# Optimization experiments

Measured on AMD Instinct MI355X. Metric: run time of the kernel, lower is better.

The kernel has to match this reference:

```python
import jax, jax.numpy as jnp
import numpy as np

N = 196608   # total bonds in batch
H = 256      # hidden_size
NH = 8       # num_heads
D = H // NH  # att_size = 32
S = 4096     # num molecules (segments)
EPS = 1e-5


def setup_inputs() -> dict:
    key = jax.random.key(0)
    ks = jax.random.split(key, 12)
    f32 = jnp.float32
    return {
        "message": jax.random.normal(ks[0], (N, H), f32),
        "W_q": jax.random.normal(ks[1], (H, H), f32) * 0.05,
        "W_k": jax.random.normal(ks[2], (H, H), f32) * 0.05,
        "W_v": jax.random.normal(ks[3], (H, H), f32) * 0.05,
        "W_r": jax.random.normal(ks[4], (D, D), f32) * 0.15,
        "w_alpha": jax.random.normal(ks[5], (D,), f32),
        "w_beta": jax.random.normal(ks[6], (D,), f32),
        "W_o": jax.random.normal(ks[7], (H, H), f32) * 0.05,
        "b_o": jax.random.normal(ks[8], (H,), f32) * 0.02,
        "gamma": 1.0 + 0.1 * jax.random.normal(ks[9], (H,), f32),
        "beta_ln": 0.1 * jax.random.normal(ks[10], (H,), f32),
        "segment_ids": jnp.sort(jax.random.randint(ks[11], (N,), 0, S, dtype=jnp.int32)),
        "num_segments": S,
    }


def reference(message, W_q, W_k, W_v, W_r, w_alpha, w_beta, W_o, b_o,
              gamma, beta_ln, segment_ids, num_segments):
    scale = D ** (-0.5)
    # projections (torch Linear: y = x @ W.T), split heads -> [N, NH, D]
    q = (message @ W_q.T).reshape(-1, NH, D)
    k = (message @ W_k.T).reshape(-1, NH, D)
    v = (message @ W_v.T).reshape(-1, NH, D)
    # additive attention: softmax over feature dim d (per bond, per head)
    alpha = jax.nn.softmax(q * w_alpha * scale, axis=-1)
    # global query: sum over bonds within each molecule -> [S, NH, D]
    gq = jax.ops.segment_sum(alpha * q, segment_ids, num_segments=num_segments)
    p = gq[segment_ids] * k                      # [N, NH, D]
    beta = jax.nn.softmax(p * w_beta * scale, axis=-1)
    gk = jax.ops.segment_sum(beta * p, segment_ids, num_segments=num_segments)
    kvi = gk[segment_ids] * v                    # key-value interaction [N, NH, D]
    out = jnp.einsum('nhd,ed->nhe', kvi, W_r) + q  # weight_r on d, residual with q
    out = jax.nn.relu(out)                       # chemprop ReLU activation; dropout p=0
    out = out.reshape(-1, NH * D)
    out = out @ W_o.T + b_o
    # LayerNorm over hidden dim
    mu = jnp.mean(out, axis=-1, keepdims=True)
    var = jnp.mean(jnp.square(out - mu), axis=-1, keepdims=True)
    out = (out - mu) * jax.lax.rsqrt(var + EPS) * gamma + beta_ln
    # prepend cached zero vector (padding row), as the torch loop does for i == 0
    zero = jnp.zeros((1, H), dtype=out.dtype)
    return jnp.concatenate([zero, out], axis=0)
```

## Files before the change

kernel.cpp:

```cpp
#include <hip/hip_runtime.h>
#include <hip/hip_bf16.h>

#define N_BONDS 196608
#define HID     256
#define NSEG    4096
#define SMSCALE 0.17677669529663687f
#define LN_EPS  1e-5f
#define CHUNK   8

typedef __hip_bfloat16 bf16;
typedef __attribute__((ext_vector_type(8))) short short8_t;
typedef __attribute__((ext_vector_type(4))) float f32x4_t;

__device__ __forceinline__ float bf2f(bf16 x) { return __bfloat162float(x); }
__device__ __forceinline__ short f2bs(float f) {
    union { bf16 b; short s; } cv; cv.b = __float2bfloat16(f); return cv.s;
}
__device__ __forceinline__ float us2f(ushort u) {
    union { ushort u; bf16 b; } cv; cv.u = u; return __bfloat162float(cv.b);
}

__device__ __forceinline__ float gsum32(float x) {
#pragma unroll
    for (int m = 16; m >= 1; m >>= 1) x += __shfl_xor(x, m);
    return x;
}

__global__ void cast_kernel(const float* __restrict__ src, ushort* __restrict__ dst, int n4) {
    int i = blockIdx.x * blockDim.x + threadIdx.x;
    const int stride = gridDim.x * blockDim.x;
    for (; i < n4; i += stride) {
        float4 v = reinterpret_cast<const float4*>(src)[i];
        union { ushort4 u; bf16 b[4]; } cv;
        cv.b[0] = __float2bfloat16(v.x);
        cv.b[1] = __float2bfloat16(v.y);
        cv.b[2] = __float2bfloat16(v.z);
        cv.b[3] = __float2bfloat16(v.w);
        reinterpret_cast<ushort4*>(dst)[i] = cv.u;
    }
}

template <typename OutT>
__global__ __launch_bounds__(256, 2) void gemm_bt(const ushort* __restrict__ A,
                                                  const ushort* __restrict__ W,
                                                  OutT* __restrict__ C) {
    __shared__ __align__(16) char lds[128 * 512];
    const int t = threadIdx.x;
    const int colhalf = blockIdx.y;
#pragma unroll
    for (int it = 0; it < 16; ++it) {
        int c = it * 256 + t;
        int j = c >> 5, kc = c & 31;
        uint4 val = *reinterpret_cast<const uint4*>(W + ((colhalf << 7) + j) * HID + (kc << 3));
        *reinterpret_cast<uint4*>(lds + j * 512 + ((kc << 4) ^ ((j & 7) << 4))) = val;
    }
    __syncthreads();

    const int wave = t >> 6, lane = t & 63;
    const int lr = lane & 15, lk = lane >> 4;
    const long rowbase = (long)blockIdx.x * 128 + wave * 32;

    f32x4_t acc[2][8];
#pragma unroll
    for (int r = 0; r < 2; ++r)
#pragma unroll
        for (int cc = 0; cc < 8; ++cc) acc[r][cc] = (f32x4_t){0.f, 0.f, 0.f, 0.f};

    const ushort* a0 = A + (rowbase + lr) * HID;
    const ushort* a1 = a0 + 16 * HID;
#pragma unroll
    for (int k0 = 0; k0 < HID; k0 += 32) {
        const int koff = k0 + lk * 8;
        short8_t af0 = *reinterpret_cast<const short8_t*>(a0 + koff);
        short8_t af1 = *reinterpret_cast<const short8_t*>(a1 + koff);
#pragma unroll
        for (int cc = 0; cc < 8; ++cc) {
            const int j = cc * 16 + lr;
            short8_t bfr = *reinterpret_cast<const short8_t*>(
                lds + j * 512 + (((k0 << 1) + (lk << 4)) ^ ((j & 7) << 4)));
            acc[0][cc] = __builtin_amdgcn_mfma_f32_16x16x32_bf16(af0, bfr, acc[0][cc], 0, 0, 0);
            acc[1][cc] = __builtin_amdgcn_mfma_f32_16x16x32_bf16(af1, bfr, acc[1][cc], 0, 0, 0);
        }
    }
#pragma unroll
    for (int r = 0; r < 2; ++r) {
#pragma unroll
        for (int cc = 0; cc < 8; ++cc) {
            const int col = (colhalf << 7) + cc * 16 + lr;
#pragma unroll
            for (int reg = 0; reg < 4; ++reg) {
                const long row = rowbase + r * 16 + lk * 4 + reg;
                const float v = acc[r][cc][reg];
                if constexpr (sizeof(OutT) == 2) C[row * HID + col] = __float2bfloat16(v);
                else                             C[row * HID + col] = v;
            }
        }
    }
}

__global__ __launch_bounds__(256) void alpha_gq_kernel(const bf16* __restrict__ qb,
                                                       const float* __restrict__ w_alpha,
                                                       const int* __restrict__ seg,
                                                       float* __restrict__ gq) {
    const int j = threadIdx.x;
    const float wa = w_alpha[j & 31] * SMSCALE;
    const long n0 = (long)blockIdx.x * CHUNK;
    float acc = 0.f;
    int cur = -1;
    for (int i = 0; i < CHUNK; ++i) {
        const long n = n0 + i;
        const int s = seg[n];
        const float qv = bf2f(qb[n * HID + j]);
        const float e = __expf(qv * wa);
        const float ssum = gsum32(e);
        const float alpha = e / ssum;
        if (s != cur) {
            if (cur >= 0) atomicAdd(&gq[(long)cur * HID + j], acc);
            acc = 0.f;
            cur = s;
        }
        acc += alpha * qv;
    }
    atomicAdd(&gq[(long)cur * HID + j], acc);
}

__global__ __launch_bounds__(256) void beta_gk_kernel(const bf16* __restrict__ kb,
                                                      const float* __restrict__ gq,
                                                      const float* __restrict__ w_beta,
                                                      const int* __restrict__ seg,
                                                      float* __restrict__ gk) {
    const int j = threadIdx.x;
    const float wb = w_beta[j & 31] * SMSCALE;
    const long n0 = (long)blockIdx.x * CHUNK;
    float acc = 0.f;
    int cur = -1;
    for (int i = 0; i < CHUNK; ++i) {
        const long n = n0 + i;
        const int s = seg[n];
        const float kv = bf2f(kb[n * HID + j]);
        const float p = gq[(long)s * HID + j] * kv;
        const float e = __expf(p * wb);
        const float ssum = gsum32(e);
        const float beta = e / ssum;
        if (s != cur) {
            if (cur >= 0) atomicAdd(&gk[(long)cur * HID + j], acc);
            acc = 0.f;
            cur = s;
        }
        acc += beta * p;
    }
    atomicAdd(&gk[(long)cur * HID + j], acc);
}

__global__ __launch_bounds__(256) void act_exact_kernel(const ushort* __restrict__ vb,
                                                        const ushort* __restrict__ qb,
                                                        const float* __restrict__ gk,
                                                        const float* __restrict__ Wr,
                                                        const int* __restrict__ seg,
                                                        ushort* __restrict__ act) {
    __shared__ __align__(16) float wr_lds[1024];
    const int t = threadIdx.x;
#pragma unroll
    for (int i = 0; i < 4; ++i) wr_lds[i * 256 + t] = Wr[i * 256 + t];
    __syncthreads();

    const long tid = (long)blockIdx.x * 256 + t;
    const int n = (int)(tid >> 3), h = (int)(tid & 7);
    const int sid = seg[n];

    const float* gp = gk + (long)sid * HID + h * 32;
    const ushort* vp = vb + tid * 32;
    float kvi[32];
#pragma unroll
    for (int dq = 0; dq < 4; ++dq) {
        short8_t v8 = *reinterpret_cast<const short8_t*>(vp + dq * 8);
        float4 ga = reinterpret_cast<const float4*>(gp)[dq * 2];
        float4 gb = reinterpret_cast<const float4*>(gp)[dq * 2 + 1];
        kvi[dq * 8 + 0] = ga.x * us2f((ushort)v8[0]);
        kvi[dq * 8 + 1] = ga.y * us2f((ushort)v8[1]);
        kvi[dq * 8 + 2] = ga.z * us2f((ushort)v8[2]);
        kvi[dq * 8 + 3] = ga.w * us2f((ushort)v8[3]);
        kvi[dq * 8 + 4] = gb.x * us2f((ushort)v8[4]);
        kvi[dq * 8 + 5] = gb.y * us2f((ushort)v8[5]);
        kvi[dq * 8 + 6] = gb.z * us2f((ushort)v8[6]);
        kvi[dq * 8 + 7] = gb.w * us2f((ushort)v8[7]);
    }

    const ushort* qp = qb + tid * 32;
    short8_t q8[4];
#pragma unroll
    for (int i = 0; i < 4; ++i) q8[i] = *reinterpret_cast<const short8_t*>(qp + i * 8);

    short8_t ob[4];
#pragma unroll
    for (int e = 0; e < 32; ++e) {
        float acc = 0.f;
        const float4* wre = reinterpret_cast<const float4*>(wr_lds + e * 32);
#pragma unroll
        for (int dq = 0; dq < 8; ++dq) {
            float4 w = wre[dq];
            acc = fmaf(kvi[dq * 4 + 0], w.x, acc);
            acc = fmaf(kvi[dq * 4 + 1], w.y, acc);
            acc = fmaf(kvi[dq * 4 + 2], w.z, acc);
            acc = fmaf(kvi[dq * 4 + 3], w.w, acc);
        }
        const float qv = us2f((ushort)q8[e >> 3][e & 7]);
        ob[e >> 3][e & 7] = f2bs(fmaxf(acc + qv, 0.f));
    }

    ushort* ap = act + tid * 32;
#pragma unroll
    for (int i = 0; i < 4; ++i) *reinterpret_cast<short8_t*>(ap + i * 8) = ob[i];
}

__global__ __launch_bounds__(256) void ln_kernel(const float* __restrict__ tmp,
                                                 const float* __restrict__ b_o,
                                                 const float* __restrict__ gamma,
                                                 const float* __restrict__ beta_ln,
                                                 float* __restrict__ out) {
    const int wave = threadIdx.x >> 6, lane = threadIdx.x & 63;
    const long row = (long)blockIdx.x * 4 + wave;
    const float4 bo = reinterpret_cast<const float4*>(b_o)[lane];
    const float4 g = reinterpret_cast<const float4*>(gamma)[lane];
    const float4 bl = reinterpret_cast<const float4*>(beta_ln)[lane];
    float4 x = reinterpret_cast<const float4*>(tmp + row * HID)[lane];
    x.x += bo.x; x.y += bo.y; x.z += bo.z; x.w += bo.w;
    float s = x.x + x.y + x.z + x.w;
#pragma unroll
    for (int m = 32; m >= 1; m >>= 1) s += __shfl_xor(s, m);
    const float mu = s * (1.f / HID);
    float4 dx = {x.x - mu, x.y - mu, x.z - mu, x.w - mu};
    float sq = dx.x * dx.x + dx.y * dx.y + dx.z * dx.z + dx.w * dx.w;
#pragma unroll
    for (int m = 32; m >= 1; m >>= 1) sq += __shfl_xor(sq, m);
    const float r = rsqrtf(sq * (1.f / HID) + LN_EPS);
    float4 o;
    o.x = dx.x * r * g.x + bl.x;
    o.y = dx.y * r * g.y + bl.y;
    o.z = dx.z * r * g.z + bl.z;
    o.w = dx.w * r * g.w + bl.w;
    reinterpret_cast<float4*>(out + (row + 1) * HID)[lane] = o;
}

extern "C" void kernel_launch(void* const* d_in, const int* in_sizes, int n_in,
                              void* d_out, int out_size, void* d_ws, size_t ws_size,
                              hipStream_t stream) {
    const float* msg    = (const float*)d_in[0];
    const float* Wq     = (const float*)d_in[1];
    const float* Wk     = (const float*)d_in[2];
    const float* Wv     = (const float*)d_in[3];
    const float* Wr     = (const float*)d_in[4];
    const float* walpha = (const float*)d_in[5];
    const float* wbeta  = (const float*)d_in[6];
    const float* Wo     = (const float*)d_in[7];
    const float* bo     = (const float*)d_in[8];
    const float* gamma  = (const float*)d_in[9];
    const float* betaln = (const float*)d_in[10];
    const int*   seg    = (const int*)d_in[11];

    char* ws = (char*)d_ws;
    const size_t nh = (size_t)N_BONDS * HID;
    size_t off = 0;
    bf16* msgb = (bf16*)(ws + off); off += nh * 2;
    bf16* qb   = (bf16*)(ws + off); off += nh * 2;
    bf16* kb   = (bf16*)(ws + off); off += nh * 2;
    bf16* vb   = (bf16*)(ws + off); off += nh * 2;
    bf16* wqb  = (bf16*)(ws + off); off += (size_t)HID * HID * 2;
    bf16* wkb  = (bf16*)(ws + off); off += (size_t)HID * HID * 2;
    bf16* wvb  = (bf16*)(ws + off); off += (size_t)HID * HID * 2;
    bf16* wob  = (bf16*)(ws + off); off += (size_t)HID * HID * 2;
    float* gq  = (float*)(ws + off); off += (size_t)NSEG * HID * 4;
    float* gk  = (float*)(ws + off); off += (size_t)NSEG * HID * 4;
    bf16*  act = msgb;
    float* tmp = (float*)qb;

    hipMemsetAsync(gq, 0, (size_t)2 * NSEG * HID * 4, stream);
    hipMemsetAsync(d_out, 0, HID * sizeof(float), stream);

    cast_kernel<<<4096, 256, 0, stream>>>(msg, (ushort*)msgb, (int)(nh / 4));
    cast_kernel<<<64, 256, 0, stream>>>(Wq, (ushort*)wqb, HID * HID / 4);
    cast_kernel<<<64, 256, 0, stream>>>(Wk, (ushort*)wkb, HID * HID / 4);
    cast_kernel<<<64, 256, 0, stream>>>(Wv, (ushort*)wvb, HID * HID / 4);
    cast_kernel<<<64, 256, 0, stream>>>(Wo, (ushort*)wob, HID * HID / 4);

    dim3 gg(N_BONDS / 128, 2);
    gemm_bt<bf16><<<gg, 256, 0, stream>>>((const ushort*)msgb, (const ushort*)wqb, qb);
    gemm_bt<bf16><<<gg, 256, 0, stream>>>((const ushort*)msgb, (const ushort*)wkb, kb);
    gemm_bt<bf16><<<gg, 256, 0, stream>>>((const ushort*)msgb, (const ushort*)wvb, vb);

    alpha_gq_kernel<<<N_BONDS / CHUNK, 256, 0, stream>>>(qb, walpha, seg, gq);
    beta_gk_kernel<<<N_BONDS / CHUNK, 256, 0, stream>>>(kb, gq, wbeta, seg, gk);

    act_exact_kernel<<<N_BONDS * 8 / 256, 256, 0, stream>>>((const ushort*)vb, (const ushort*)qb,
                                                            gk, Wr, seg, (ushort*)act);

    gemm_bt<float><<<gg, 256, 0, stream>>>((const ushort*)act, (const ushort*)wob, tmp);
    ln_kernel<<<N_BONDS / 4, 256, 0, stream>>>(tmp, bo, gamma, betaln, (float*)d_out);
}
```

Baseline: 626.8 us.

## Fuse fp32-to-bf16 casts into GEMMs, use MFMA for W_r, store tmp in bf16

```diff
diff --git a/kernel.cpp b/kernel.cpp
--- a/kernel.cpp
+++ b/kernel.cpp
@@ -1,5 +1,6 @@
 #include <hip/hip_runtime.h>
 #include <hip/hip_bf16.h>
+#include <type_traits>
 
 #define N_BONDS 196608
 #define HID     256
@@ -26,23 +27,9 @@
     return x;
 }
 
-__global__ void cast_kernel(const float* __restrict__ src, ushort* __restrict__ dst, int n4) {
-    int i = blockIdx.x * blockDim.x + threadIdx.x;
-    const int stride = gridDim.x * blockDim.x;
-    for (; i < n4; i += stride) {
-        float4 v = reinterpret_cast<const float4*>(src)[i];
-        union { ushort4 u; bf16 b[4]; } cv;
-        cv.b[0] = __float2bfloat16(v.x);
-        cv.b[1] = __float2bfloat16(v.y);
-        cv.b[2] = __float2bfloat16(v.z);
-        cv.b[3] = __float2bfloat16(v.w);
-        reinterpret_cast<ushort4*>(dst)[i] = cv.u;
-    }
-}
-
-template <typename OutT>
-__global__ __launch_bounds__(256, 2) void gemm_bt(const ushort* __restrict__ A,
-                                                  const ushort* __restrict__ W,
+template <typename AT, typename OutT>
+__global__ __launch_bounds__(256, 2) void gemm_bt(const AT* __restrict__ A,
+                                                  const float* __restrict__ W,
                                                   OutT* __restrict__ C) {
     __shared__ __align__(16) char lds[128 * 512];
     const int t = threadIdx.x;
@@ -51,8 +38,13 @@
     for (int it = 0; it < 16; ++it) {
         int c = it * 256 + t;
         int j = c >> 5, kc = c & 31;
-        uint4 val = *reinterpret_cast<const uint4*>(W + ((colhalf << 7) + j) * HID + (kc << 3));
-        *reinterpret_cast<uint4*>(lds + j * 512 + ((kc << 4) ^ ((j & 7) << 4))) = val;
+        const float* wp = W + ((colhalf << 7) + j) * HID + (kc << 3);
+        float4 w0 = *reinterpret_cast<const float4*>(wp);
+        float4 w1 = *reinterpret_cast<const float4*>(wp + 4);
+        union { uint4 u; short s[8]; } cv;
+        cv.s[0] = f2bs(w0.x); cv.s[1] = f2bs(w0.y); cv.s[2] = f2bs(w0.z); cv.s[3] = f2bs(w0.w);
+        cv.s[4] = f2bs(w1.x); cv.s[5] = f2bs(w1.y); cv.s[6] = f2bs(w1.z); cv.s[7] = f2bs(w1.w);
+        *reinterpret_cast<uint4*>(lds + j * 512 + ((kc << 4) ^ ((j & 7) << 4))) = cv.u;
     }
     __syncthreads();
 
@@ -66,13 +58,25 @@
 #pragma unroll
         for (int cc = 0; cc < 8; ++cc) acc[r][cc] = (f32x4_t){0.f, 0.f, 0.f, 0.f};
 
-    const ushort* a0 = A + (rowbase + lr) * HID;
-    const ushort* a1 = a0 + 16 * HID;
+    const AT* a0 = A + (rowbase + lr) * HID;
+    const AT* a1 = a0 + 16 * HID;
 #pragma unroll
     for (int k0 = 0; k0 < HID; k0 += 32) {
         const int koff = k0 + lk * 8;
-        short8_t af0 = *reinterpret_cast<const short8_t*>(a0 + koff);
-        short8_t af1 = *reinterpret_cast<const short8_t*>(a1 + koff);
+        short8_t af0, af1;
+        if constexpr (std::is_same_v<AT, float>) {
+            float4 x0 = *reinterpret_cast<const float4*>(a0 + koff);
+            float4 x1 = *reinterpret_cast<const float4*>(a0 + koff + 4);
+            float4 y0 = *reinterpret_cast<const float4*>(a1 + koff);
+            float4 y1 = *reinterpret_cast<const float4*>(a1 + koff + 4);
+            af0[0] = f2bs(x0.x); af0[1] = f2bs(x0.y); af0[2] = f2bs(x0.z); af0[3] = f2bs(x0.w);
+            af0[4] = f2bs(x1.x); af0[5] = f2bs(x1.y); af0[6] = f2bs(x1.z); af0[7] = f2bs(x1.w);
+            af1[0] = f2bs(y0.x); af1[1] = f2bs(y0.y); af1[2] = f2bs(y0.z); af1[3] = f2bs(y0.w);
+            af1[4] = f2bs(y1.x); af1[5] = f2bs(y1.y); af1[6] = f2bs(y1.z); af1[7] = f2bs(y1.w);
+        } else {
+            af0 = *reinterpret_cast<const short8_t*>(a0 + koff);
+            af1 = *reinterpret_cast<const short8_t*>(a1 + koff);
+        }
 #pragma unroll
         for (int cc = 0; cc < 8; ++cc) {
             const int j = cc * 16 + lr;
@@ -152,68 +156,73 @@
     atomicAdd(&gk[(long)cur * HID + j], acc);
 }
 
-__global__ __launch_bounds__(256) void act_exact_kernel(const ushort* __restrict__ vb,
-                                                        const ushort* __restrict__ qb,
-                                                        const float* __restrict__ gk,
-                                                        const float* __restrict__ Wr,
-                                                        const int* __restrict__ seg,
-                                                        ushort* __restrict__ act) {
-    __shared__ __align__(16) float wr_lds[1024];
+__global__ __launch_bounds__(256) void act_mfma_kernel(const ushort* __restrict__ vb,
+                                                       const ushort* __restrict__ qb,
+                                                       const float* __restrict__ gk,
+                                                       const float* __restrict__ Wr,
+                                                       const int* __restrict__ seg,
+                                                       ushort* __restrict__ act) {
     const int t = threadIdx.x;
-#pragma unroll
-    for (int i = 0; i < 4; ++i) wr_lds[i * 256 + t] = Wr[i * 256 + t];
-    __syncthreads();
-
-    const long tid = (long)blockIdx.x * 256 + t;
-    const int n = (int)(tid >> 3), h = (int)(tid & 7);
-    const int sid = seg[n];
-
-    const float* gp = gk + (long)sid * HID + h * 32;
-    const ushort* vp = vb + tid * 32;
-    float kvi[32];
-#pragma unroll
-    for (int dq = 0; dq < 4; ++dq) {
-        short8_t v8 = *reinterpret_cast<const short8_t*>(vp + dq * 8);
-        float4 ga = reinterpret_cast<const float4*>(gp)[dq * 2];
-        float4 gb = reinterpret_cast<const float4*>(gp)[dq * 2 + 1];
-        kvi[dq * 8 + 0] = ga.x * us2f((ushort)v8[0]);
-        kvi[dq * 8 + 1] = ga.y * us2f((ushort)v8[1]);
-        kvi[dq * 8 + 2] = ga.z * us2f((ushort)v8[2]);
-        kvi[dq * 8 + 3] = ga.w * us2f((ushort)v8[3]);
-        kvi[dq * 8 + 4] = gb.x * us2f((ushort)v8[4]);
-        kvi[dq * 8 + 5] = gb.y * us2f((ushort)v8[5]);
-        kvi[dq * 8 + 6] = gb.z * us2f((ushort)v8[6]);
-        kvi[dq * 8 + 7] = gb.w * us2f((ushort)v8[7]);
-    }
-
-    const ushort* qp = qb + tid * 32;
-    short8_t q8[4];
-#pragma unroll
-    for (int i = 0; i < 4; ++i) q8[i] = *reinterpret_cast<const short8_t*>(qp + i * 8);
-
-    short8_t ob[4];
-#pragma unroll
-    for (int e = 0; e < 32; ++e) {
-        float acc = 0.f;
-        const float4* wre = reinterpret_cast<const float4*>(wr_lds + e * 32);
-#pragma unroll
-        for (int dq = 0; dq < 8; ++dq) {
-            float4 w = wre[dq];
-            acc = fmaf(kvi[dq * 4 + 0], w.x, acc);
-            acc = fmaf(kvi[dq * 4 + 1], w.y, acc);
-            acc = fmaf(kvi[dq * 4 + 2], w.z, acc);
-            acc = fmaf(kvi[dq * 4 + 3], w.w, acc);
-        }
-        const float qv = us2f((ushort)q8[e >> 3][e & 7]);
-        ob[e >> 3][e & 7] = f2bs(fmaxf(acc + qv, 0.f));
-    }
-
-    ushort* ap = act + tid * 32;
-#pragma unroll
-    for (int i = 0; i < 4; ++i) *reinterpret_cast<short8_t*>(ap + i * 8) = ob[i];
-}
-
-__global__ __launch_bounds__(256) void ln_kernel(const float* __restrict__ tmp,
+    const int wave = t >> 6, lane = t & 63;
+    const int lr = lane & 15, lk = lane >> 4;
+
+    short8_t bhi[2], blo[2];
+#pragma unroll
+    for (int ct = 0; ct < 2; ++ct) {
+        const float* wr = Wr + (ct * 16 + lr) * 32 + lk * 8;
+#pragma unroll
+        for (int e = 0; e < 8; ++e) {
+            const float w = wr[e];
+            const short h = f2bs(w);
+            bhi[ct][e] = h;
+            blo[ct][e] = f2bs(w - us2f((ushort)h));
+        }
+    }
+
+    const long rowblock = (long)blockIdx.x * 256 + wave * 64;
+#pragma unroll
+    for (int rt = 0; rt < 4; ++rt) {
+        const long rtbase = rowblock + rt * 16;
+        const long arow = rtbase + lr;
+        const int n = (int)(arow >> 3), h = (int)(arow & 7);
+        const int sid = seg[n];
+        short8_t v8 = *reinterpret_cast<const short8_t*>(vb + arow * 32 + lk * 8);
+        const float* gp = gk + (long)sid * HID + h * 32 + lk * 8;
+        float4 g0 = *reinterpret_cast<const float4*>(gp);
+        float4 g1 = *reinterpret_cast<const float4*>(gp + 4);
+        float kvi[8];
+        kvi[0] = g0.x * us2f((ushort)v8[0]);
+        kvi[1] = g0.y * us2f((ushort)v8[1]);
+        kvi[2] = g0.z * us2f((ushort)v8[2]);
+        kvi[3] = g0.w * us2f((ushort)v8[3]);
+        kvi[4] = g1.x * us2f((ushort)v8[4]);
+        kvi[5] = g1.y * us2f((ushort)v8[5]);
+        kvi[6] = g1.z * us2f((ushort)v8[6]);
+        kvi[7] = g1.w * us2f((ushort)v8[7]);
+        short8_t ahi, alo;
+#pragma unroll
+        for (int e = 0; e < 8; ++e) {
+            const short hh = f2bs(kvi[e]);
+            ahi[e] = hh;
+            alo[e] = f2bs(kvi[e] - us2f((ushort)hh));
+        }
+#pragma unroll
+        for (int ct = 0; ct < 2; ++ct) {
+            f32x4_t c = (f32x4_t){0.f, 0.f, 0.f, 0.f};
+            c = __builtin_amdgcn_mfma_f32_16x16x32_bf16(ahi, bhi[ct], c, 0, 0, 0);
+            c = __builtin_amdgcn_mfma_f32_16x16x32_bf16(alo, bhi[ct], c, 0, 0, 0);
+            c = __builtin_amdgcn_mfma_f32_16x16x32_bf16(ahi, blo[ct], c, 0, 0, 0);
+#pragma unroll
+            for (int reg = 0; reg < 4; ++reg) {
+                const long row = rtbase + lk * 4 + reg;
+                const long idx = row * 32 + ct * 16 + lr;
+                act[idx] = (ushort)f2bs(fmaxf(c[reg] + us2f(qb[idx]), 0.f));
+            }
+        }
+    }
+}
+
+__global__ __launch_bounds__(256) void ln_kernel(const ushort* __restrict__ tmp,
                                                  const float* __restrict__ b_o,
                                                  const float* __restrict__ gamma,
                                                  const float* __restrict__ beta_ln,
@@ -223,8 +232,8 @@
     const float4 bo = reinterpret_cast<const float4*>(b_o)[lane];
     const float4 g = reinterpret_cast<const float4*>(gamma)[lane];
     const float4 bl = reinterpret_cast<const float4*>(beta_ln)[lane];
-    float4 x = reinterpret_cast<const float4*>(tmp + row * HID)[lane];
-    x.x += bo.x; x.y += bo.y; x.z += bo.z; x.w += bo.w;
+    const ushort4 xr = reinterpret_cast<const ushort4*>(tmp + row * HID)[lane];
+    float4 x = {us2f(xr.x) + bo.x, us2f(xr.y) + bo.y, us2f(xr.z) + bo.z, us2f(xr.w) + bo.w};
     float s = x.x + x.y + x.z + x.w;
 #pragma unroll
     for (int m = 32; m >= 1; m >>= 1) s += __shfl_xor(s, m);
@@ -261,39 +270,28 @@
     char* ws = (char*)d_ws;
     const size_t nh = (size_t)N_BONDS * HID;
     size_t off = 0;
-    bf16* msgb = (bf16*)(ws + off); off += nh * 2;
+    bf16* act  = (bf16*)(ws + off); off += nh * 2;
     bf16* qb   = (bf16*)(ws + off); off += nh * 2;
     bf16* kb   = (bf16*)(ws + off); off += nh * 2;
     bf16* vb   = (bf16*)(ws + off); off += nh * 2;
-    bf16* wqb  = (bf16*)(ws + off); off += (size_t)HID * HID * 2;
-    bf16* wkb  = (bf16*)(ws + off); off += (size_t)HID * HID * 2;
-    bf16* wvb  = (bf16*)(ws + off); off += (size_t)HID * HID * 2;
-    bf16* wob  = (bf16*)(ws + off); off += (size_t)HID * HID * 2;
     float* gq  = (float*)(ws + off); off += (size_t)NSEG * HID * 4;
     float* gk  = (float*)(ws + off); off += (size_t)NSEG * HID * 4;
-    bf16*  act = msgb;
-    float* tmp = (float*)qb;
+    bf16*  tmp = qb;
 
     hipMemsetAsync(gq, 0, (size_t)2 * NSEG * HID * 4, stream);
     hipMemsetAsync(d_out, 0, HID * sizeof(float), stream);
 
-    cast_kernel<<<4096, 256, 0, stream>>>(msg, (ushort*)msgb, (int)(nh / 4));
-    cast_kernel<<<64, 256, 0, stream>>>(Wq, (ushort*)wqb, HID * HID / 4);
-    cast_kernel<<<64, 256, 0, stream>>>(Wk, (ushort*)wkb, HID * HID / 4);
-    cast_kernel<<<64, 256, 0, stream>>>(Wv, (ushort*)wvb, HID * HID / 4);
-    cast_kernel<<<64, 256, 0, stream>>>(Wo, (ushort*)wob, HID * HID / 4);
-
     dim3 gg(N_BONDS / 128, 2);
-    gemm_bt<bf16><<<gg, 256, 0, stream>>>((const ushort*)msgb, (const ushort*)wqb, qb);
-    gemm_bt<bf16><<<gg, 256, 0, stream>>>((const ushort*)msgb, (const ushort*)wkb, kb);
-    gemm_bt<bf16><<<gg, 256, 0, stream>>>((const ushort*)msgb, (const ushort*)wvb, vb);
+    gemm_bt<float, bf16><<<gg, 256, 0, stream>>>(msg, Wq, qb);
+    gemm_bt<float, bf16><<<gg, 256, 0, stream>>>(msg, Wk, kb);
+    gemm_bt<float, bf16><<<gg, 256, 0, stream>>>(msg, Wv, vb);
 
     alpha_gq_kernel<<<N_BONDS / CHUNK, 256, 0, stream>>>(qb, walpha, seg, gq);
     beta_gk_kernel<<<N_BONDS / CHUNK, 256, 0, stream>>>(kb, gq, wbeta, seg, gk);
 
-    act_exact_kernel<<<N_BONDS * 8 / 256, 256, 0, stream>>>((const ushort*)vb, (const ushort*)qb,
-                                                            gk, Wr, seg, (ushort*)act);
-
-    gemm_bt<float><<<gg, 256, 0, stream>>>((const ushort*)act, (const ushort*)wob, tmp);
-    ln_kernel<<<N_BONDS / 4, 256, 0, stream>>>(tmp, bo, gamma, betaln, (float*)d_out);
-}
+    act_mfma_kernel<<<N_BONDS * 8 / 256, 256, 0, stream>>>((const ushort*)vb, (const ushort*)qb,
+                                                           gk, Wr, seg, (ushort*)act);
+
+    gemm_bt<ushort, bf16><<<gg, 256, 0, stream>>>((const ushort*)act, Wo, tmp);
+    ln_kernel<<<N_BONDS / 4, 256, 0, stream>>>((const ushort*)tmp, bo, gamma, betaln, (float*)d_out);
+}
```

Measured after the change: 662.8 us. +5.7%, slower.
